# Optimization experiments

Hardware: AMD Instinct MI355X
Metric: run time of the kernel (lower is better)

The kernel has to match this reference:

```python
import jax, jax.numpy as jnp
import numpy as np


def setup_inputs() -> dict:
    key = jax.random.key(0)
    k1, k2 = jax.random.split(key)
    # NCHW input activations
    x = jax.random.normal(k1, (32, 256, 56, 56), dtype=jnp.float32)
    # OIHW weight; centered small-uniform so sign() is +/-1 with equal probability
    # (torch init is rand()*0.001, all-positive, which would make sign degenerate
    #  for kernel testing; magnitude scale kept comparable)
    weight = (jax.random.uniform(k2, (256, 256, 3, 3), dtype=jnp.float32) - 0.5) * 0.002
    return {"x": x, "weight": weight}


def reference(x, weight):
    # per-output-channel scaling factor: mean |w| over (in, kh, kw), detached
    scale = jax.lax.stop_gradient(
        jnp.mean(jnp.abs(weight), axis=(1, 2, 3), keepdims=True)
    )  # [O,1,1,1]
    w_clip = jnp.clip(weight, -1.0, 1.0)
    # STE: forward value = scale * sign(w); gradient flows through clip(w)
    binary_w = jax.lax.stop_gradient(scale * jnp.sign(weight) - w_clip) + w_clip
    y = jax.lax.conv_general_dilated(
        x,
        binary_w,
        window_strides=(1, 1),
        padding=((1, 1), (1, 1)),
        dimension_numbers=("NCHW", "OIHW", "NCHW"),
        feature_group_count=1,
    )
    return y
```

## Files before the change

kernel.cpp:

```cpp
#include <hip/hip_runtime.h>
#include <stdint.h>

typedef __attribute__((ext_vector_type(8))) short bf16x8;
typedef __attribute__((ext_vector_type(4))) float f32x4;

#define N_IMG 32
#define CI 256
#define CO 256
#define HH_ 56
#define WW_ 56
#define HP 58
#define WP 58
#define SPP (HP*WP)
#define SPI (HH_*WW_)

#define XB_BYTES ((size_t)N_IMG*SPP*CI*2)
#define W2_OFF   XB_BYTES
#define W2_BYTES ((size_t)9*CO*CI*2)
#define SCALE_OFF (W2_OFF + W2_BYTES)

__device__ __forceinline__ unsigned int pack_bf16(float a, float b) {
  unsigned int u0 = __builtin_bit_cast(unsigned int, a);
  unsigned int u1 = __builtin_bit_cast(unsigned int, b);
  u0 = (u0 + 0x7fffu + ((u0 >> 16) & 1u)) >> 16;
  u1 = (u1 + 0x7fffu + ((u1 >> 16) & 1u)) >> 16;
  return u0 | (u1 << 16);
}

__device__ __forceinline__ void gl_lds16(const void* g, void* l) {
  __builtin_amdgcn_global_load_lds(
      (const __attribute__((address_space(1))) unsigned int*)g,
      (__attribute__((address_space(3))) unsigned int*)l, 16, 0, 0);
}

__global__ __launch_bounds__(256) void border_zero_k(unsigned short* __restrict__ xb) {
  int gid = blockIdx.x*256 + threadIdx.x;
  int cell = gid >> 5, part = gid & 31;
  int n = cell / 228, b = cell - n*228;
  int h, w;
  if (b < 58)       { h = 0;          w = b;        }
  else if (b < 116) { h = 57;         w = b - 58;   }
  else if (b < 172) { h = b - 116 + 1; w = 0;       }
  else              { h = b - 172 + 1; w = 57;      }
  uint4 z = make_uint4(0u,0u,0u,0u);
  *(uint4*)&xb[((size_t)n*SPP + (size_t)h*WP + w)*CI + part*8] = z;
}

__global__ __launch_bounds__(256) void nchw2nhwc_k(const float* __restrict__ x,
                                                   unsigned short* __restrict__ xb) {
  __shared__ float tile[64*64];
  int bid = blockIdx.x;
  int n = bid / 196; int r = bid - n*196;
  int cb = r / 49;   int t0 = (r - cb*49) * 64;
  int t = threadIdx.x;
  int row = t >> 4, l16 = t & 15;
  const float* src = x + ((size_t)(n*CI + cb*64))*SPI + t0;
#pragma unroll
  for (int it = 0; it < 4; ++it) {
    int c = it*16 + row;
    float4 v = *(const float4*)&src[(size_t)c*SPI + l16*4];
    const float* vf = (const float*)&v;
#pragma unroll
    for (int j = 0; j < 4; ++j) {
      int sp = l16*4 + j;
      int cs = c ^ (((sp >> 2) & 7) << 3);
      tile[sp*64 + cs] = vf[j];
    }
  }
  __syncthreads();
#pragma unroll
  for (int it = 0; it < 2; ++it) {
    int u = it*256 + t;
    int sp = u >> 3, part = u & 7;
    int g = (part*8) ^ (((sp >> 2) & 7) << 3);
    float4 f0 = *(const float4*)&tile[sp*64 + g];
    float4 f1 = *(const float4*)&tile[sp*64 + g + 4];
    const float* a0 = (const float*)&f0; const float* a1 = (const float*)&f1;
    uint4 pk;
    pk.x = pack_bf16(a0[0], a0[1]);
    pk.y = pack_bf16(a0[2], a0[3]);
    pk.z = pack_bf16(a1[0], a1[1]);
    pk.w = pack_bf16(a1[2], a1[3]);
    int spg = t0 + sp; int h = spg / 56; int w = spg - h*56;
    size_t psp = (size_t)(h+1)*WP + (w+1);
    *(uint4*)&xb[((size_t)n*SPP + psp)*CI + cb*64 + part*8] = pk;
  }
}

__global__ __launch_bounds__(256) void prep_w_k(const float* __restrict__ wt,
                                                unsigned short* __restrict__ w2,
                                                float* __restrict__ scale) {
  int o = blockIdx.x; int t = threadIdx.x;
  const float* wr = wt + (size_t)o*2304 + t*9;
  float s = 0.f;
#pragma unroll
  for (int tap = 0; tap < 9; ++tap) {
    float v = wr[tap];
    s += fabsf(v);
    unsigned short sg = (v > 0.f) ? (unsigned short)0x3F80u
                       : ((v < 0.f) ? (unsigned short)0xBF80u : (unsigned short)0u);
    w2[((size_t)tap*CO + o)*CI + t] = sg;
  }
  __shared__ float red[4];
#pragma unroll
  for (int off = 32; off > 0; off >>= 1) s += __shfl_down(s, off, 64);
  if ((t & 63) == 0) red[t >> 6] = s;
  __syncthreads();
  if (t == 0) scale[o] = (red[0]+red[1]+red[2]+red[3]) * (1.0f/2304.0f);
}

#define PCH 1280
__global__ __launch_bounds__(256, 2) void binconv_k(
    const unsigned short* __restrict__ xb,
    const unsigned short* __restrict__ w2,
    const float* __restrict__ scale,
    float* __restrict__ out) {
  __shared__ unsigned short sp_buf[2][PCH*8];

  int bid = blockIdx.x;
  int orig = (bid & 7)*112 + (bid >> 3);
  int ot = orig & 1, pt = orig >> 1;
  int n = pt / 14, rem = pt - n*14;
  int ht = rem >> 1, wtl = rem & 1;
  int h0 = ht*8, w0 = wtl*28, OB = ot*128;
  int tid = threadIdx.x;
  int lane = tid & 63, wid = tid >> 6;
  int wo = wid >> 1, wp = wid & 1;
  int lrow = lane & 15, lgrp = lane >> 4;

  int pb[7];
#pragma unroll
  for (int f = 0; f < 7; ++f) {
    int p = wp*112 + f*16 + lrow;
    int th = p / 28; int tw = p - th*28;
    pb[f] = (th*30 + tw)*32 + lgrp*8;
  }

  const unsigned short* wA = w2 + (((size_t)(OB + wo*64 + lrow)) << 8) + lgrp*8;

  const unsigned short* xsrc = xb + ((size_t)n*SPP + (size_t)h0*WP + w0)*CI;

  f32x4 acc[4][7];
#pragma unroll
  for (int m = 0; m < 4; ++m)
#pragma unroll
    for (int f = 0; f < 7; ++f) {
      f32x4 z = {0.f, 0.f, 0.f, 0.f};
      acc[m][f] = z;
    }

#define STAGE(BUF, CC)                                                        \
  {                                                                           \
    const unsigned short* g_ = xsrc + (CC)*32;                                \
    _Pragma("unroll")                                                         \
    for (int rdi = 0; rdi < 5; ++rdi) {                                       \
      int u = rdi*256 + tid;                                                  \
      if (u < 1200) {                                                         \
        int rr = u >> 2, cg = u & 3;                                          \
        int hh = rr / 30, ww = rr - hh*30;                                    \
        gl_lds16(g_ + ((size_t)hh*WP + ww)*CI + cg*8,                         \
                 &sp_buf[BUF][(size_t)(rdi*256 + (tid & ~63))*8]);            \
      }                                                                       \
    }                                                                         \
  }

  STAGE(0, 0);
  __syncthreads();

  for (int cc = 0; cc < 8; ++cc) {
    int cur = cc & 1;
    if (cc < 7) STAGE(cur ^ 1, cc + 1);

    const unsigned short* aCC = wA + cc*32;
#pragma unroll
    for (int tap = 0; tap < 9; ++tap) {
      const int dh = tap / 3, dw = tap - dh*3;
      const int toff = (dh*30 + dw)*32;
      const unsigned short* aP = aCC + ((size_t)tap << 16);
      bf16x8 a0 = *(const bf16x8*)(aP);
      bf16x8 a1 = *(const bf16x8*)(aP + 4096);
      bf16x8 a2 = *(const bf16x8*)(aP + 8192);
      bf16x8 a3 = *(const bf16x8*)(aP + 12288);
      bf16x8 bv[7];
#pragma unroll
      for (int f = 0; f < 7; ++f)
        bv[f] = *(const bf16x8*)&sp_buf[cur][pb[f] + toff];
#pragma unroll
      for (int f = 0; f < 7; ++f) {
        acc[0][f] = __builtin_amdgcn_mfma_f32_16x16x32_bf16(a0, bv[f], acc[0][f], 0, 0, 0);
        acc[1][f] = __builtin_amdgcn_mfma_f32_16x16x32_bf16(a1, bv[f], acc[1][f], 0, 0, 0);
        acc[2][f] = __builtin_amdgcn_mfma_f32_16x16x32_bf16(a2, bv[f], acc[2][f], 0, 0, 0);
        acc[3][f] = __builtin_amdgcn_mfma_f32_16x16x32_bf16(a3, bv[f], acc[3][f], 0, 0, 0);
      }
    }
    __syncthreads();
  }

  float sc[4][4];
#pragma unroll
  for (int m = 0; m < 4; ++m)
#pragma unroll
    for (int r = 0; r < 4; ++r)
      sc[m][r] = scale[OB + wo*64 + m*16 + lgrp*4 + r];

#pragma unroll
  for (int f = 0; f < 7; ++f) {
    int p = wp*112 + f*16 + lrow;
    int th = p / 28; int tw = p - th*28;
    size_t spo = (size_t)(h0+th)*WW_ + (w0+tw);
#pragma unroll
    for (int m = 0; m < 4; ++m) {
      int o = OB + wo*64 + m*16 + lgrp*4;
      float* dst = out + ((size_t)n*CO + o)*SPI + spo;
#pragma unroll
      for (int r = 0; r < 4; ++r)
        dst[(size_t)r*SPI] = acc[m][f][r] * sc[m][r];
    }
  }
}

extern "C" void kernel_launch(void* const* d_in, const int* in_sizes, int n_in,
                              void* d_out, int out_size, void* d_ws, size_t ws_size,
                              hipStream_t stream) {
  const float* x  = (const float*)d_in[0];
  const float* wt = (const float*)d_in[1];
  float* out = (float*)d_out;
  unsigned short* xb = (unsigned short*)d_ws;
  unsigned short* w2 = (unsigned short*)((char*)d_ws + W2_OFF);
  float* scale = (float*)((char*)d_ws + SCALE_OFF);

  border_zero_k<<<912, 256, 0, stream>>>(xb);
  nchw2nhwc_k<<<6272, 256, 0, stream>>>(x, xb);
  prep_w_k<<<256, 256, 0, stream>>>(wt, w2, scale);
  binconv_k<<<896, 256, 0, stream>>>(xb, w2, scale, out);
}
```

Baseline: 346.3 us.

## Switch binary conv to 32x32x16 MFMA with padded LDS and register-staged prefetch

Measured after the change: 363.5 us. +5.0%, slower.

```diff
diff --git a/kernel.cpp b/kernel.cpp
--- a/kernel.cpp
+++ b/kernel.cpp
@@ -2,7 +2,7 @@
 #include <stdint.h>
 
 typedef __attribute__((ext_vector_type(8))) short bf16x8;
-typedef __attribute__((ext_vector_type(4))) float f32x4;
+typedef __attribute__((ext_vector_type(16))) float f32x16;
 
 #define N_IMG 32
 #define CI 256
@@ -19,18 +19,14 @@
 #define W2_BYTES ((size_t)9*CO*CI*2)
 #define SCALE_OFF (W2_OFF + W2_BYTES)
 
+#define KCP 40
+
 __device__ __forceinline__ unsigned int pack_bf16(float a, float b) {
   unsigned int u0 = __builtin_bit_cast(unsigned int, a);
   unsigned int u1 = __builtin_bit_cast(unsigned int, b);
   u0 = (u0 + 0x7fffu + ((u0 >> 16) & 1u)) >> 16;
   u1 = (u1 + 0x7fffu + ((u1 >> 16) & 1u)) >> 16;
   return u0 | (u1 << 16);
-}
-
-__device__ __forceinline__ void gl_lds16(const void* g, void* l) {
-  __builtin_amdgcn_global_load_lds(
-      (const __attribute__((address_space(1))) unsigned int*)g,
-      (__attribute__((address_space(3))) unsigned int*)l, 16, 0, 0);
 }
 
 __global__ __launch_bounds__(256) void border_zero_k(unsigned short* __restrict__ xb) {
@@ -92,6 +88,7 @@
                                                 float* __restrict__ scale) {
   int o = blockIdx.x; int t = threadIdx.x;
   const float* wr = wt + (size_t)o*2304 + t*9;
+  int cc = t >> 5, ks = (t >> 4) & 1, chi = t & 15;
   float s = 0.f;
 #pragma unroll
   for (int tap = 0; tap < 9; ++tap) {
@@ -99,7 +96,7 @@
     s += fabsf(v);
     unsigned short sg = (v > 0.f) ? (unsigned short)0x3F80u
                        : ((v < 0.f) ? (unsigned short)0xBF80u : (unsigned short)0u);
-    w2[((size_t)tap*CO + o)*CI + t] = sg;
+    w2[(size_t)(tap*16 + cc*2 + ks)*4096 + o*16 + chi] = sg;
   }
   __shared__ float red[4];
 #pragma unroll
@@ -109,13 +106,12 @@
   if (t == 0) scale[o] = (red[0]+red[1]+red[2]+red[3]) * (1.0f/2304.0f);
 }
 
-#define PCH 1280
 __global__ __launch_bounds__(256, 2) void binconv_k(
     const unsigned short* __restrict__ xb,
     const unsigned short* __restrict__ w2,
     const float* __restrict__ scale,
     float* __restrict__ out) {
-  __shared__ unsigned short sp_buf[2][PCH*8];
+  __shared__ unsigned short sp_buf[2][300*KCP];
 
   int bid = blockIdx.x;
   int orig = (bid & 7)*112 + (bid >> 3);
@@ -125,96 +121,94 @@
   int h0 = ht*8, w0 = wtl*28, OB = ot*128;
   int tid = threadIdx.x;
   int lane = tid & 63, wid = tid >> 6;
-  int wo = wid >> 1, wp = wid & 1;
-  int lrow = lane & 15, lgrp = lane >> 4;
+  int l31 = lane & 31, hi = lane >> 5;
 
   int pb[7];
 #pragma unroll
   for (int f = 0; f < 7; ++f) {
-    int p = wp*112 + f*16 + lrow;
-    int th = p / 28; int tw = p - th*28;
-    pb[f] = (th*30 + tw)*32 + lgrp*8;
-  }
-
-  const unsigned short* wA = w2 + (((size_t)(OB + wo*64 + lrow)) << 8) + lgrp*8;
+    int px = f*32 + l31;
+    int th = px / 28; int tw = px - th*28;
+    pb[f] = (th*30 + tw)*KCP + hi*8;
+  }
+
+  const unsigned short* wA = w2 + (size_t)(OB + wid*32)*16 + (l31*16 + hi*8);
 
   const unsigned short* xsrc = xb + ((size_t)n*SPP + (size_t)h0*WP + w0)*CI;
 
-  f32x4 acc[4][7];
-#pragma unroll
-  for (int m = 0; m < 4; ++m)
-#pragma unroll
-    for (int f = 0; f < 7; ++f) {
-      f32x4 z = {0.f, 0.f, 0.f, 0.f};
-      acc[m][f] = z;
-    }
-
-#define STAGE(BUF, CC)                                                        \
-  {                                                                           \
-    const unsigned short* g_ = xsrc + (CC)*32;                                \
-    _Pragma("unroll")                                                         \
-    for (int rdi = 0; rdi < 5; ++rdi) {                                       \
-      int u = rdi*256 + tid;                                                  \
-      if (u < 1200) {                                                         \
-        int rr = u >> 2, cg = u & 3;                                          \
-        int hh = rr / 30, ww = rr - hh*30;                                    \
-        gl_lds16(g_ + ((size_t)hh*WP + ww)*CI + cg*8,                         \
-                 &sp_buf[BUF][(size_t)(rdi*256 + (tid & ~63))*8]);            \
-      }                                                                       \
-    }                                                                         \
-  }
-
-  STAGE(0, 0);
+  int goff[5], loff[5]; bool sact[5];
+#pragma unroll
+  for (int rdi = 0; rdi < 5; ++rdi) {
+    int u = rdi*256 + tid;
+    sact[rdi] = (u < 1200);
+    int px = u >> 2, g = u & 3;
+    int hh = px / 30, ww = px - hh*30;
+    goff[rdi] = (hh*WP + ww)*CI + g*8;
+    loff[rdi] = px*KCP + g*8;
+  }
+
+  f32x16 acc[7];
+#pragma unroll
+  for (int f = 0; f < 7; ++f)
+#pragma unroll
+    for (int r = 0; r < 16; ++r) acc[f][r] = 0.f;
+
+  uint4 st[5];
+#pragma unroll
+  for (int rdi = 0; rdi < 5; ++rdi)
+    if (sact[rdi]) st[rdi] = *(const uint4*)&xsrc[goff[rdi]];
+#pragma unroll
+  for (int rdi = 0; rdi < 5; ++rdi)
+    if (sact[rdi]) *(uint4*)&sp_buf[0][loff[rdi]] = st[rdi];
   __syncthreads();
 
+  int cur = 0;
   for (int cc = 0; cc < 8; ++cc) {
-    int cur = cc & 1;
-    if (cc < 7) STAGE(cur ^ 1, cc + 1);
-
-    const unsigned short* aCC = wA + cc*32;
+    if (cc < 7) {
+#pragma unroll
+      for (int rdi = 0; rdi < 5; ++rdi)
+        if (sact[rdi]) st[rdi] = *(const uint4*)&xsrc[goff[rdi] + (cc+1)*32];
+    }
+    const unsigned short* aCC = wA + (size_t)(cc*2)*4096;
+    const unsigned short* sbuf = sp_buf[cur];
 #pragma unroll
     for (int tap = 0; tap < 9; ++tap) {
       const int dh = tap / 3, dw = tap - dh*3;
-      const int toff = (dh*30 + dw)*32;
-      const unsigned short* aP = aCC + ((size_t)tap << 16);
-      bf16x8 a0 = *(const bf16x8*)(aP);
-      bf16x8 a1 = *(const bf16x8*)(aP + 4096);
-      bf16x8 a2 = *(const bf16x8*)(aP + 8192);
-      bf16x8 a3 = *(const bf16x8*)(aP + 12288);
-      bf16x8 bv[7];
-#pragma unroll
-      for (int f = 0; f < 7; ++f)
-        bv[f] = *(const bf16x8*)&sp_buf[cur][pb[f] + toff];
-#pragma unroll
-      for (int f = 0; f < 7; ++f) {
-        acc[0][f] = __builtin_amdgcn_mfma_f32_16x16x32_bf16(a0, bv[f], acc[0][f], 0, 0, 0);
-        acc[1][f] = __builtin_amdgcn_mfma_f32_16x16x32_bf16(a1, bv[f], acc[1][f], 0, 0, 0);
-        acc[2][f] = __builtin_amdgcn_mfma_f32_16x16x32_bf16(a2, bv[f], acc[2][f], 0, 0, 0);
-        acc[3][f] = __builtin_amdgcn_mfma_f32_16x16x32_bf16(a3, bv[f], acc[3][f], 0, 0, 0);
+      const int toff = (dh*30 + dw)*KCP;
+#pragma unroll
+      for (int ks = 0; ks < 2; ++ks) {
+        bf16x8 a = *(const bf16x8*)(aCC + (size_t)(tap*16 + ks)*4096);
+        bf16x8 bv[7];
+#pragma unroll
+        for (int f = 0; f < 7; ++f)
+          bv[f] = *(const bf16x8*)&sbuf[pb[f] + toff + ks*16];
+#pragma unroll
+        for (int f = 0; f < 7; ++f)
+          acc[f] = __builtin_amdgcn_mfma_f32_32x32x16_bf16(a, bv[f], acc[f], 0, 0, 0);
       }
     }
-    __syncthreads();
-  }
-
-  float sc[4][4];
-#pragma unroll
-  for (int m = 0; m < 4; ++m)
-#pragma unroll
-    for (int r = 0; r < 4; ++r)
-      sc[m][r] = scale[OB + wo*64 + m*16 + lgrp*4 + r];
+    if (cc < 7) {
+#pragma unroll
+      for (int rdi = 0; rdi < 5; ++rdi)
+        if (sact[rdi]) *(uint4*)&sp_buf[cur ^ 1][loff[rdi]] = st[rdi];
+      __syncthreads();
+      cur ^= 1;
+    }
+  }
+
+  float sc_[16];
+#pragma unroll
+  for (int r = 0; r < 16; ++r)
+    sc_[r] = scale[OB + wid*32 + (r & 3) + 8*(r >> 2) + 4*hi];
 
 #pragma unroll
   for (int f = 0; f < 7; ++f) {
-    int p = wp*112 + f*16 + lrow;
-    int th = p / 28; int tw = p - th*28;
+    int px = f*32 + l31;
+    int th = px / 28; int tw = px - th*28;
     size_t spo = (size_t)(h0+th)*WW_ + (w0+tw);
 #pragma unroll
-    for (int m = 0; m < 4; ++m) {
-      int o = OB + wo*64 + m*16 + lgrp*4;
-      float* dst = out + ((size_t)n*CO + o)*SPI + spo;
-#pragma unroll
-      for (int r = 0; r < 4; ++r)
-        dst[(size_t)r*SPI] = acc[m][f][r] * sc[m][r];
+    for (int r = 0; r < 16; ++r) {
+      int o = OB + wid*32 + (r & 3) + 8*(r >> 2) + 4*hi;
+      out[((size_t)n*CO + o)*SPI + spo] = acc[f][r] * sc_[r];
     }
   }
 }
```
